# Kernel tuning notes

Measured on AMD Instinct MI355X. Metric: run time of the kernel, lower is better.

The kernel has to match this reference:

```python
import jax, jax.numpy as jnp
import numpy as np

B, D, H = 65536, 32, 128


def setup_inputs() -> dict:
    key = jax.random.key(0)
    ks = jax.random.split(key, 6)
    return {
        "x": jax.random.normal(ks[0], (B, 1, D), dtype=jnp.float32),
        "W1": jax.random.normal(ks[1], (D, H), dtype=jnp.float32) * (1.0 / np.sqrt(D)),
        "b1": jax.random.normal(ks[2], (H,), dtype=jnp.float32) * 0.01,
        "W2": jax.random.normal(ks[3], (H, D), dtype=jnp.float32) * (1.0 / np.sqrt(H)),
        "b2": jax.random.normal(ks[4], (D,), dtype=jnp.float32) * 0.01,
        "theta_0": jnp.array([0.5], dtype=jnp.float32),
    }


def reference(x, W1, b1, W2, b2, theta_0):
    # x: (B, 1, D). Network u: D -> H -> D with tanh (transformation=none, no bounds).
    xf = x[:, 0, :]  # (B, D)

    def u_fn(xv):  # (D,) -> (D,)
        h = jnp.tanh(xv @ W1 + b1)
        return h @ W2 + b2

    # div u = trace of per-sample Jacobian, computed in ONE vectorized forward-mode
    # sweep (replaces the per-dimension torch.autograd.grad loop).
    div_u = jax.vmap(lambda xv: jnp.trace(jax.jacfwd(u_fn)(xv)))(xf)  # (B,)

    u_x = jax.vmap(u_fn)(xf)  # (B, D)
    grad_log_pi = -xf  # standard normal: grad log pi(x) = -x, shape (B, D)
    grad_log_pi_u = jnp.sum(grad_log_pi * u_x, axis=-1)  # (B,)  == (B,1,D)@(B,D,1) flattened

    out = (grad_log_pi_u + div_u + theta_0)[:, None]  # (B, 1)
    return out
```

## Files before the change

### kernel.cpp

```cpp
#include <hip/hip_runtime.h>


#define NROWS 65536
#define DD 32
#define HH 128
#define NTILE 25

typedef __attribute__((ext_vector_type(8))) short short8;
typedef __attribute__((ext_vector_type(4))) float f32x4;

static __device__ __forceinline__ unsigned short f2bf(float f) {
    unsigned u = __float_as_uint(f);
    u += 0x7fff + ((u >> 16) & 1);
    return (unsigned short)(u >> 16);
}
static __device__ __forceinline__ float bf2f(unsigned short h) {
    return __uint_as_float(((unsigned)h) << 16);
}

__global__ __launch_bounds__(256, 5) void stein_fused(
    const float* __restrict__ x, const float* __restrict__ W1,
    const float* __restrict__ b1, const float* __restrict__ W2,
    const float* __restrict__ b2, const float* __restrict__ theta,
    float* __restrict__ out) {
    __shared__ unsigned short lb[NTILE * 512];
    __shared__ float2 cb[HH];

    const int tid = threadIdx.x;
    const int lane = tid & 63;
    const int wv = tid >> 6;
    const int quad = lane >> 4;
    const int cl = lane & 15;
    const int rowbase = blockIdx.x * 64 + wv * 16;

    const float* xr = x + (size_t)(rowbase + cl) * DD + quad * 8;
    const float4 x0 = *(const float4*)xr;
    const float4 x1 = *(const float4*)(xr + 4);

    if (tid < 128) {
        const int n = tid;
        const int t = n >> 4, cc = n & 15;
#pragma unroll
        for (int kg = 0; kg < 4; ++kg) {
            short8 hi, lo;
#pragma unroll
            for (int j = 0; j < 8; ++j) {
                const float w = W1[(kg * 8 + j) * HH + n];
                const unsigned short h = f2bf(w);
                hi[j] = (short)h;
                lo[j] = (short)f2bf(w - bf2f(h));
            }
            *(short8*)(lb + t * 512 + (kg * 16 + cc) * 8) = hi;
            *(short8*)(lb + (8 + t) * 512 + (kg * 16 + cc) * 8) = lo;
        }
    } else {
        const int n = tid - 128;
        const int t2 = 16 + (n >> 4), cc = n & 15;
        float row[DD];
        const float4* wr = (const float4*)(W2 + n * DD);
#pragma unroll
        for (int q = 0; q < 8; ++q) {
            const float4 f = wr[q];
            row[4 * q + 0] = f.x; row[4 * q + 1] = f.y;
            row[4 * q + 2] = f.z; row[4 * q + 3] = f.w;
        }
#pragma unroll
        for (int g = 0; g < 4; ++g) {
            short8 v;
#pragma unroll
            for (int j = 0; j < 8; ++j) v[j] = (short)f2bf(row[g * 8 + j]);
            *(short8*)(lb + t2 * 512 + (g * 16 + cc) * 8) = v;
        }
        float acc = 0.f;
#pragma unroll
        for (int k = 0; k < DD; ++k) acc = fmaf(W1[k * HH + n], row[k], acc);
        cb[n] = make_float2(acc, b1[n]);
        if (n < 16) {
#pragma unroll
            for (int g = 0; g < 4; ++g) {
                short8 v;
#pragma unroll
                for (int j = 0; j < 8; ++j)
                    v[j] = (n == 0) ? (short)f2bf(b2[g * 8 + j]) : (short)0;
                *(short8*)(lb + 24 * 512 + (g * 16 + n) * 8) = v;
            }
        }
    }
    __syncthreads();

    const float xv[8] = {x0.x, x0.y, x0.z, x0.w, x1.x, x1.y, x1.z, x1.w};
    short8 aHi, aLo;
#pragma unroll
    for (int j = 0; j < 8; ++j) {
        const unsigned short h = f2bf(xv[j]);
        aHi[j] = (short)h;
        aLo[j] = (short)f2bf(xv[j] - bf2f(h));
    }

    const f32x4 zero = {0.f, 0.f, 0.f, 0.f};
    float sa[4] = {0.f, 0.f, 0.f, 0.f};

#pragma unroll
    for (int t = 0; t < 8; ++t) {
        const short8 bH = *(const short8*)(lb + t * 512 + lane * 8);
        const short8 bL = *(const short8*)(lb + (8 + t) * 512 + lane * 8);
        const short8 bW = *(const short8*)(lb + (16 + t) * 512 + lane * 8);
        const float2 cbv = cb[t * 16 + cl];
        f32x4 z = zero;
        z = __builtin_amdgcn_mfma_f32_16x16x32_bf16(aLo, bH, z, 0, 0, 0);
        z = __builtin_amdgcn_mfma_f32_16x16x32_bf16(aHi, bL, z, 0, 0, 0);
        z = __builtin_amdgcn_mfma_f32_16x16x32_bf16(aHi, bH, z, 0, 0, 0);
        const f32x4 v = __builtin_amdgcn_mfma_f32_16x16x32_bf16(aHi, bW, zero, 0, 0, 0);
#pragma unroll
        for (int r = 0; r < 4; ++r) {
            const float zz = z[r] + cbv.y;
            const float e = __expf(2.f * zz);
            const float h = fmaf(-2.f, __builtin_amdgcn_rcpf(e + 1.f), 1.f);
            sa[r] += cbv.x - h * fmaf(h, cbv.x, v[r]);
        }
    }
    {
        const short8 bW = *(const short8*)(lb + 24 * 512 + lane * 8);
        const f32x4 v = __builtin_amdgcn_mfma_f32_16x16x32_bf16(aHi, bW, zero, 0, 0, 0);
#pragma unroll
        for (int r = 0; r < 4; ++r) sa[r] -= v[r];
    }

#pragma unroll
    for (int r = 0; r < 4; ++r) {
#pragma unroll
        for (int m = 1; m < 16; m <<= 1) sa[r] += __shfl_xor(sa[r], m, 64);
    }

    if (cl == 0) {
        const float th = theta[0];
        float4 o;
        o.x = sa[0] + th;
        o.y = sa[1] + th;
        o.z = sa[2] + th;
        o.w = sa[3] + th;
        *(float4*)(out + rowbase + quad * 4) = o;
    }
}

extern "C" void kernel_launch(void* const* d_in, const int* in_sizes, int n_in,
                              void* d_out, int out_size, void* d_ws, size_t ws_size,
                              hipStream_t stream) {
    const float* x = (const float*)d_in[0];
    const float* W1 = (const float*)d_in[1];
    const float* b1 = (const float*)d_in[2];
    const float* W2 = (const float*)d_in[3];
    const float* b2 = (const float*)d_in[4];
    const float* theta = (const float*)d_in[5];
    float* out = (float*)d_out;

    stein_fused<<<NROWS / 64, 256, 0, stream>>>(x, W1, b1, W2, b2, theta, out);
}
```

Measured before the change: 73.16 us.

## Split weight preprocessing into a one-block prep kernel with global workspace

Moves the bf16 hi/lo weight splitting and the W1·W2 diagonal precompute out of every block into a single-block prep kernel. The prep kernel writes to the workspace, and the main kernel reads the packed tiles straight from global memory (through cache) instead of LDS. This removes redundant per-block conversion work and the __syncthreads barrier. In exchange it adds a second, serialized launch and replaces LDS reads with global/L2 reads inside the MFMA loop.

```diff
diff --git a/kernel.cpp b/kernel.cpp
--- a/kernel.cpp
+++ b/kernel.cpp
@@ -18,25 +18,11 @@
     return __uint_as_float(((unsigned)h) << 16);
 }
 
-__global__ __launch_bounds__(256, 5) void stein_fused(
-    const float* __restrict__ x, const float* __restrict__ W1,
-    const float* __restrict__ b1, const float* __restrict__ W2,
-    const float* __restrict__ b2, const float* __restrict__ theta,
-    float* __restrict__ out) {
-    __shared__ unsigned short lb[NTILE * 512];
-    __shared__ float2 cb[HH];
-
+__global__ __launch_bounds__(256) void stein_prep(
+    const float* __restrict__ W1, const float* __restrict__ b1,
+    const float* __restrict__ W2, const float* __restrict__ b2,
+    float2* __restrict__ cbw, unsigned short* __restrict__ lbw) {
     const int tid = threadIdx.x;
-    const int lane = tid & 63;
-    const int wv = tid >> 6;
-    const int quad = lane >> 4;
-    const int cl = lane & 15;
-    const int rowbase = blockIdx.x * 64 + wv * 16;
-
-    const float* xr = x + (size_t)(rowbase + cl) * DD + quad * 8;
-    const float4 x0 = *(const float4*)xr;
-    const float4 x1 = *(const float4*)(xr + 4);
-
     if (tid < 128) {
         const int n = tid;
         const int t = n >> 4, cc = n & 15;
@@ -50,8 +36,8 @@
                 hi[j] = (short)h;
                 lo[j] = (short)f2bf(w - bf2f(h));
             }
-            *(short8*)(lb + t * 512 + (kg * 16 + cc) * 8) = hi;
-            *(short8*)(lb + (8 + t) * 512 + (kg * 16 + cc) * 8) = lo;
+            *(short8*)(lbw + t * 512 + (kg * 16 + cc) * 8) = hi;
+            *(short8*)(lbw + (8 + t) * 512 + (kg * 16 + cc) * 8) = lo;
         }
     } else {
         const int n = tid - 128;
@@ -69,12 +55,12 @@
             short8 v;
 #pragma unroll
             for (int j = 0; j < 8; ++j) v[j] = (short)f2bf(row[g * 8 + j]);
-            *(short8*)(lb + t2 * 512 + (g * 16 + cc) * 8) = v;
+            *(short8*)(lbw + t2 * 512 + (g * 16 + cc) * 8) = v;
         }
         float acc = 0.f;
 #pragma unroll
         for (int k = 0; k < DD; ++k) acc = fmaf(W1[k * HH + n], row[k], acc);
-        cb[n] = make_float2(acc, b1[n]);
+        cbw[n] = make_float2(acc, b1[n]);
         if (n < 16) {
 #pragma unroll
             for (int g = 0; g < 4; ++g) {
@@ -82,11 +68,26 @@
 #pragma unroll
                 for (int j = 0; j < 8; ++j)
                     v[j] = (n == 0) ? (short)f2bf(b2[g * 8 + j]) : (short)0;
-                *(short8*)(lb + 24 * 512 + (g * 16 + n) * 8) = v;
+                *(short8*)(lbw + 24 * 512 + (g * 16 + n) * 8) = v;
             }
         }
     }
-    __syncthreads();
+}
+
+__global__ __launch_bounds__(256, 4) void stein_main(
+    const float* __restrict__ x, const float* __restrict__ theta,
+    const float2* __restrict__ cbw, const unsigned short* __restrict__ lbw,
+    float* __restrict__ out) {
+    const int tid = threadIdx.x;
+    const int lane = tid & 63;
+    const int wv = tid >> 6;
+    const int quad = lane >> 4;
+    const int cl = lane & 15;
+    const int rowbase = blockIdx.x * 64 + wv * 16;
+
+    const float* xr = x + (size_t)(rowbase + cl) * DD + quad * 8;
+    const float4 x0 = *(const float4*)xr;
+    const float4 x1 = *(const float4*)(xr + 4);
 
     const float xv[8] = {x0.x, x0.y, x0.z, x0.w, x1.x, x1.y, x1.z, x1.w};
     short8 aHi, aLo;
@@ -99,13 +100,14 @@
 
     const f32x4 zero = {0.f, 0.f, 0.f, 0.f};
     float sa[4] = {0.f, 0.f, 0.f, 0.f};
+    const unsigned short* lbl = lbw + lane * 8;
 
 #pragma unroll
     for (int t = 0; t < 8; ++t) {
-        const short8 bH = *(const short8*)(lb + t * 512 + lane * 8);
-        const short8 bL = *(const short8*)(lb + (8 + t) * 512 + lane * 8);
-        const short8 bW = *(const short8*)(lb + (16 + t) * 512 + lane * 8);
-        const float2 cbv = cb[t * 16 + cl];
+        const short8 bH = *(const short8*)(lbl + t * 512);
+        const short8 bL = *(const short8*)(lbl + (8 + t) * 512);
+        const short8 bW = *(const short8*)(lbl + (16 + t) * 512);
+        const float2 cbv = cbw[t * 16 + cl];
         f32x4 z = zero;
         z = __builtin_amdgcn_mfma_f32_16x16x32_bf16(aLo, bH, z, 0, 0, 0);
         z = __builtin_amdgcn_mfma_f32_16x16x32_bf16(aHi, bL, z, 0, 0, 0);
@@ -120,7 +122,7 @@
         }
     }
     {
-        const short8 bW = *(const short8*)(lb + 24 * 512 + lane * 8);
+        const short8 bW = *(const short8*)(lbl + 24 * 512);
         const f32x4 v = __builtin_amdgcn_mfma_f32_16x16x32_bf16(aHi, bW, zero, 0, 0, 0);
 #pragma unroll
         for (int r = 0; r < 4; ++r) sa[r] -= v[r];
@@ -154,5 +156,9 @@
     const float* theta = (const float*)d_in[5];
     float* out = (float*)d_out;
 
-    stein_fused<<<NROWS / 64, 256, 0, stream>>>(x, W1, b1, W2, b2, theta, out);
+    float2* cbw = (float2*)d_ws;
+    unsigned short* lbw = (unsigned short*)((char*)d_ws + 1024);
+
+    stein_prep<<<1, 256, 0, stream>>>(W1, b1, W2, b2, cbw, lbw);
+    stein_main<<<NROWS / 64, 256, 0, stream>>>(x, theta, cbw, lbw, out);
 }
```

Result: no change. 74.12 us (+1.3%).
